# Kernel tuning notes

Hardware: AMD Instinct MI355X
Metric: run time of the kernel (lower is better)

Reference implementation:

```python
import jax, jax.numpy as jnp
import numpy as np

PAD = 0

def setup_inputs() -> dict:
    key = jax.random.key(0)
    k1, k2, k3, k4 = jax.random.split(key, 4)
    B, S, F, V, H, D = 64, 256, 4, 50257, 768, 512
    words = jax.random.randint(k1, (B, S, F), 0, V, dtype=jnp.int64)  # pad_index=0 occurs rarely at random
    E = jax.random.normal(k2, (V, H), dtype=jnp.float32) * 0.02      # stand-in for transformer last_hidden_state producer
    W = jax.random.normal(k3, (H, D), dtype=jnp.float32) * 0.02      # FFN projection weight
    b = jax.random.normal(k4, (D,), dtype=jnp.float32) * 0.02
    return {"words": words, "E": E, "W": W, "b": b}

def reference(words, E, W, b):
    # words: [B, S, F] subword ids; mask out pad subwords
    mask = (words != PAD)                                  # [B,S,F] bool
    sub = E[words] * mask[..., None].astype(E.dtype)       # [B,S,F,H], pads zeroed
    cnt = mask.sum(-1).astype(E.dtype)                     # [B,S] subwords per word
    # segment-mean over the fix_len axis; fully-padded words -> 0 (matches pad_sequence(..., 0))
    word_emb = sub.sum(-2) / jnp.maximum(cnt, 1.0)[..., None]   # [B,S,H]
    word_emb = jnp.where((cnt > 0)[..., None], word_emb, 0.0)
    return word_emb @ W + b                                # [B,S,D]
```

## Files before the change

### kernel.cpp

```cpp
#include <hip/hip_runtime.h>
#include <hip/hip_bf16.h>

#define M_TOT 16384
#define K_TOT 768
#define N_TOT 512
#define BM 16
#define NT 12
#define NSLOT 96

typedef __attribute__((ext_vector_type(8))) __bf16 bf16x8;
typedef __attribute__((ext_vector_type(4))) float f32x4;

static __device__ __forceinline__ ushort f2bf(float x) {
  union { float f; unsigned int u; } v; v.f = x;
  unsigned int r = v.u + 0x7fffu + ((v.u >> 16) & 1u);
  return (ushort)(r >> 16);
}
static __device__ __forceinline__ unsigned pack2(float lo, float hi) {
  return (unsigned)f2bf(lo) | ((unsigned)f2bf(hi) << 16);
}

__global__ __launch_bounds__(256) void wt_kernel(const float* __restrict__ W,
                                                 ushort* __restrict__ Wt) {
  __shared__ float tile[64][65];
  const int t  = threadIdx.x;
  const int k0 = blockIdx.x * 64;
  const int n0 = blockIdx.y * 64;
#pragma unroll
  for (int i = 0; i < 4; ++i) {
    const int idx = t + i * 256;
    const int r = idx >> 4;
    const int c = (idx & 15) * 4;
    const float4 v =
        *reinterpret_cast<const float4*>(W + (size_t)(k0 + r) * N_TOT + n0 + c);
    tile[r][c + 0] = v.x; tile[r][c + 1] = v.y;
    tile[r][c + 2] = v.z; tile[r][c + 3] = v.w;
  }
  __syncthreads();
#pragma unroll
  for (int i = 0; i < 4; ++i) {
    const int idx = t + i * 256;
    const int rn = idx >> 4;
    const int ck = (idx & 15) * 4;
    ushort4 o;
    o.x = f2bf(tile[ck + 0][rn]);
    o.y = f2bf(tile[ck + 1][rn]);
    o.z = f2bf(tile[ck + 2][rn]);
    o.w = f2bf(tile[ck + 3][rn]);
    const int kg    = k0 + ck;
    const int chunk = kg >> 3;
    const int e0    = kg & 7;
    *reinterpret_cast<ushort4*>(
        &Wt[((size_t)chunk * N_TOT + n0 + rn) * 8 + e0]) = o;
  }
}

__global__ __launch_bounds__(256) void fused_kernel(
    const int* __restrict__ words, const float* __restrict__ E,
    const ushort* __restrict__ Wt, const float* __restrict__ bias,
    float* __restrict__ out) {
  __shared__ ushort A_l[BM * NSLOT * 8];
  __shared__ int   eoff_l[BM][4];
  __shared__ float msk_l[BM][4];
  __shared__ float scl_l[BM];

  const int t    = threadIdx.x;
  const int lane = t & 63;
  const int w    = t >> 6;
  const int bm   = blockIdx.x;

  if (t < BM) {
    const int4 w4 =
        *reinterpret_cast<const int4*>(words + (size_t)(bm * BM + t) * 4);
    const int ids[4] = {w4.x, w4.y, w4.z, w4.w};
    float cnt = 0.f;
#pragma unroll
    for (int f = 0; f < 4; ++f) {
      eoff_l[t][f] = ids[f] * K_TOT;
      const float m = (ids[f] != 0) ? 1.f : 0.f;
      msk_l[t][f] = m;
      cnt += m;
    }
    scl_l[t] = (cnt > 0.f) ? (1.f / cnt) : 0.f;
  }
  __syncthreads();

  const int sr  = t >> 4;
  const int c16 = t & 15;
  const float4* pf[4];
#pragma unroll
  for (int f = 0; f < 4; ++f)
    pf[f] = reinterpret_cast<const float4*>(E + eoff_l[sr][f]);
  const float m0 = msk_l[sr][0], m1 = msk_l[sr][1];
  const float m2 = msk_l[sr][2], m3 = msk_l[sr][3];
  const float scl = scl_l[sr];

  float4 vgA[8], vgB[8];

#define G_LOAD(vg, g)                                                        \
  do {                                                                       \
    const int s_ = c16 + 16 * (g);                                           \
    _Pragma("unroll") for (int f = 0; f < 4; ++f) {                          \
      vg[2 * f + 0] = pf[f][s_ * 2 + 0];                                     \
      vg[2 * f + 1] = pf[f][s_ * 2 + 1];                                     \
    }                                                                        \
  } while (0)

#define G_MATH(vg, g)                                                        \
  do {                                                                       \
    const int s_  = c16 + 16 * (g);                                          \
    const int kt_ = s_ >> 3;                                                 \
    const int sw_ = (s_ & 7) ^ (sr & 7);                                     \
    float s[8];                                                              \
    _Pragma("unroll") for (int j = 0; j < 4; ++j) {                          \
      s[j] = (vg[0][j] * m0 + vg[2][j] * m1 + vg[4][j] * m2 + vg[6][j] * m3) \
             * scl;                                                          \
      s[4 + j] =                                                             \
          (vg[1][j] * m0 + vg[3][j] * m1 + vg[5][j] * m2 + vg[7][j] * m3) *  \
          scl;                                                               \
    }                                                                        \
    uint4 o;                                                                 \
    o.x = pack2(s[0], s[1]); o.y = pack2(s[2], s[3]);                        \
    o.z = pack2(s[4], s[5]); o.w = pack2(s[6], s[7]);                        \
    *reinterpret_cast<uint4*>(                                               \
        &A_l[(sr * NSLOT + kt_ * 8 + sw_) * 8]) = o;                         \
  } while (0)

  G_LOAD(vgA, 0);  G_LOAD(vgB, 1);
  G_MATH(vgA, 0);  G_LOAD(vgA, 2);
  G_MATH(vgB, 1);  G_LOAD(vgB, 3);
  G_MATH(vgA, 2);  G_LOAD(vgA, 4);
  G_MATH(vgB, 3);  G_LOAD(vgB, 5);
  G_MATH(vgA, 4);
  G_MATH(vgB, 5);
#undef G_LOAD
#undef G_MATH
  __syncthreads();

  f32x4 acc[8];
#pragma unroll
  for (int n = 0; n < 8; ++n) acc[n] = (f32x4){0.f, 0.f, 0.f, 0.f};

  const int rsel = lane & 15;
  const int ksel = lane >> 4;
  const int colBase = w * 128 + rsel;

#pragma unroll
  for (int kt = 0; kt < NT; ++kt) {
#pragma unroll
    for (int kk = 0; kk < 2; ++kk) {
      const int ks = kk * 4 + ksel;
      const bf16x8 af = *reinterpret_cast<const bf16x8*>(
          &A_l[(rsel * NSLOT + kt * 8 + (ks ^ (rsel & 7))) * 8]);
      bf16x8 bfr[8];
#pragma unroll
      for (int n = 0; n < 8; ++n)
        bfr[n] = *reinterpret_cast<const bf16x8*>(
            &Wt[((size_t)(kt * 8 + ks) * N_TOT + colBase + n * 16) * 8]);
      __builtin_amdgcn_s_setprio(1);
#pragma unroll
      for (int n = 0; n < 8; ++n)
        acc[n] = __builtin_amdgcn_mfma_f32_16x16x32_bf16(af, bfr[n], acc[n],
                                                         0, 0, 0);
      __builtin_amdgcn_s_setprio(0);
    }
  }

  const int row0 = bm * BM + (ksel << 2);
#pragma unroll
  for (int n = 0; n < 8; ++n) {
    const float bv = bias[colBase + n * 16];
#pragma unroll
    for (int j = 0; j < 4; ++j) {
      __builtin_nontemporal_store(
          acc[n][j] + bv,
          &out[(size_t)(row0 + j) * N_TOT + colBase + n * 16]);
    }
  }
}

extern "C" void kernel_launch(void* const* d_in, const int* in_sizes, int n_in,
                              void* d_out, int out_size, void* d_ws,
                              size_t ws_size, hipStream_t stream) {
  const int*   words = (const int*)d_in[0];
  const float* E     = (const float*)d_in[1];
  const float* W     = (const float*)d_in[2];
  const float* b     = (const float*)d_in[3];
  float* out = (float*)d_out;

  ushort* Wtws = (ushort*)d_ws;

  hipLaunchKernelGGL(wt_kernel, dim3(K_TOT / 64, N_TOT / 64), dim3(256), 0,
                     stream, W, Wtws);
  hipLaunchKernelGGL(fused_kernel, dim3(M_TOT / BM), dim3(256), 0, stream,
                     words, E, Wtws, b, out);
}
```

Before: 64.41 us.

## Enlarge row tile to 64 with 512-thread blocks for W fragment reuse

Raises the M tile from 16 to 64 rows and doubles the block to 8 waves. The gather is reorganised so each wave loads 8 full embedding rows with lane-contiguous float4 reads. In the GEMM each wave computes a 64x64 output tile, using 4x4 MFMA accumulators. Each loaded W fragment is now reused across four row tiles, which cuts global and L2 traffic for Wt. In exchange the grid shrinks to 256 blocks and LDS use grows to about 96KB per block, which limits residency and may leave fewer gather loads in flight to hide latency.

```diff
diff --git a/kernel.cpp b/kernel.cpp
--- a/kernel.cpp
+++ b/kernel.cpp
@@ -4,9 +4,8 @@
 #define M_TOT 16384
 #define K_TOT 768
 #define N_TOT 512
-#define BM 16
+#define BM 64
 #define NT 12
-#define NSLOT 96
 
 typedef __attribute__((ext_vector_type(8))) __bf16 bf16x8;
 typedef __attribute__((ext_vector_type(4))) float f32x4;
@@ -55,11 +54,11 @@
   }
 }
 
-__global__ __launch_bounds__(256) void fused_kernel(
+__global__ __launch_bounds__(512, 2) void fused_kernel(
     const int* __restrict__ words, const float* __restrict__ E,
     const ushort* __restrict__ Wt, const float* __restrict__ bias,
     float* __restrict__ out) {
-  __shared__ ushort A_l[BM * NSLOT * 8];
+  __shared__ ushort A_l[BM * 96 * 8];
   __shared__ int   eoff_l[BM][4];
   __shared__ float msk_l[BM][4];
   __shared__ float scl_l[BM];
@@ -85,96 +84,103 @@
   }
   __syncthreads();
 
-  const int sr  = t >> 4;
-  const int c16 = t & 15;
-  const float4* pf[4];
-#pragma unroll
-  for (int f = 0; f < 4; ++f)
-    pf[f] = reinterpret_cast<const float4*>(E + eoff_l[sr][f]);
-  const float m0 = msk_l[sr][0], m1 = msk_l[sr][1];
-  const float m2 = msk_l[sr][2], m3 = msk_l[sr][3];
-  const float scl = scl_l[sr];
-
-  float4 vgA[8], vgB[8];
-
-#define G_LOAD(vg, g)                                                        \
+  const int rbase = w * 8;
+  float4 vA[12], vB[12];
+
+#define G_LOAD(vv, r)                                                        \
   do {                                                                       \
-    const int s_ = c16 + 16 * (g);                                           \
+    const int row_ = rbase + (r);                                            \
     _Pragma("unroll") for (int f = 0; f < 4; ++f) {                          \
-      vg[2 * f + 0] = pf[f][s_ * 2 + 0];                                     \
-      vg[2 * f + 1] = pf[f][s_ * 2 + 1];                                     \
+      const float4* p_ =                                                     \
+          reinterpret_cast<const float4*>(E + eoff_l[row_][f]) + lane;       \
+      vv[f * 3 + 0] = p_[0];                                                 \
+      vv[f * 3 + 1] = p_[64];                                                \
+      vv[f * 3 + 2] = p_[128];                                               \
     }                                                                        \
   } while (0)
 
-#define G_MATH(vg, g)                                                        \
+#define G_MATH(vv, r)                                                        \
   do {                                                                       \
-    const int s_  = c16 + 16 * (g);                                          \
-    const int kt_ = s_ >> 3;                                                 \
-    const int sw_ = (s_ & 7) ^ (sr & 7);                                     \
-    float s[8];                                                              \
-    _Pragma("unroll") for (int j = 0; j < 4; ++j) {                          \
-      s[j] = (vg[0][j] * m0 + vg[2][j] * m1 + vg[4][j] * m2 + vg[6][j] * m3) \
-             * scl;                                                          \
-      s[4 + j] =                                                             \
-          (vg[1][j] * m0 + vg[3][j] * m1 + vg[5][j] * m2 + vg[7][j] * m3) *  \
-          scl;                                                               \
+    const int row_ = rbase + (r);                                            \
+    const float km0 = msk_l[row_][0], km1 = msk_l[row_][1];                  \
+    const float km2 = msk_l[row_][2], km3 = msk_l[row_][3];                  \
+    const float ksc = scl_l[row_];                                           \
+    _Pragma("unroll") for (int c = 0; c < 3; ++c) {                          \
+      float s[4];                                                            \
+      _Pragma("unroll") for (int j = 0; j < 4; ++j)                          \
+        s[j] = (vv[0 * 3 + c][j] * km0 + vv[1 * 3 + c][j] * km1 +            \
+                vv[2 * 3 + c][j] * km2 + vv[3 * 3 + c][j] * km3) * ksc;      \
+      uint2 o_;                                                              \
+      o_.x = pack2(s[0], s[1]);                                              \
+      o_.y = pack2(s[2], s[3]);                                              \
+      const int slot_ = c * 32 + ((lane >> 1) ^ (r));   \
+      *reinterpret_cast<uint2*>(                                             \
+          &A_l[row_ * 768 + slot_ * 8 + (lane & 1) * 4]) = o_;               \
     }                                                                        \
-    uint4 o;                                                                 \
-    o.x = pack2(s[0], s[1]); o.y = pack2(s[2], s[3]);                        \
-    o.z = pack2(s[4], s[5]); o.w = pack2(s[6], s[7]);                        \
-    *reinterpret_cast<uint4*>(                                               \
-        &A_l[(sr * NSLOT + kt_ * 8 + sw_) * 8]) = o;                         \
   } while (0)
 
-  G_LOAD(vgA, 0);  G_LOAD(vgB, 1);
-  G_MATH(vgA, 0);  G_LOAD(vgA, 2);
-  G_MATH(vgB, 1);  G_LOAD(vgB, 3);
-  G_MATH(vgA, 2);  G_LOAD(vgA, 4);
-  G_MATH(vgB, 3);  G_LOAD(vgB, 5);
-  G_MATH(vgA, 4);
-  G_MATH(vgB, 5);
+  G_LOAD(vA, 0);  G_LOAD(vB, 1);
+  G_MATH(vA, 0);  G_LOAD(vA, 2);
+  G_MATH(vB, 1);  G_LOAD(vB, 3);
+  G_MATH(vA, 2);  G_LOAD(vA, 4);
+  G_MATH(vB, 3);  G_LOAD(vB, 5);
+  G_MATH(vA, 4);  G_LOAD(vA, 6);
+  G_MATH(vB, 5);  G_LOAD(vB, 7);
+  G_MATH(vA, 6);
+  G_MATH(vB, 7);
 #undef G_LOAD
 #undef G_MATH
   __syncthreads();
 
-  f32x4 acc[8];
-#pragma unroll
-  for (int n = 0; n < 8; ++n) acc[n] = (f32x4){0.f, 0.f, 0.f, 0.f};
+  f32x4 acc[4][4];
+#pragma unroll
+  for (int m = 0; m < 4; ++m)
+#pragma unroll
+    for (int n = 0; n < 4; ++n) acc[m][n] = (f32x4){0.f, 0.f, 0.f, 0.f};
 
   const int rsel = lane & 15;
   const int ksel = lane >> 4;
-  const int colBase = w * 128 + rsel;
+  const int colBase = w * 64 + rsel;
 
 #pragma unroll
   for (int kt = 0; kt < NT; ++kt) {
 #pragma unroll
     for (int kk = 0; kk < 2; ++kk) {
-      const int ks = kk * 4 + ksel;
-      const bf16x8 af = *reinterpret_cast<const bf16x8*>(
-          &A_l[(rsel * NSLOT + kt * 8 + (ks ^ (rsel & 7))) * 8]);
-      bf16x8 bfr[8];
-#pragma unroll
-      for (int n = 0; n < 8; ++n)
+      const int g = kt * 8 + kk * 4 + ksel;
+      bf16x8 af[4], bfr[4];
+#pragma unroll
+      for (int m = 0; m < 4; ++m) {
+        const int r_ = m * 16 + rsel;
+        af[m] = *reinterpret_cast<const bf16x8*>(
+            &A_l[r_ * 768 + (g ^ (r_ & 7)) * 8]);
+      }
+#pragma unroll
+      for (int n = 0; n < 4; ++n)
         bfr[n] = *reinterpret_cast<const bf16x8*>(
-            &Wt[((size_t)(kt * 8 + ks) * N_TOT + colBase + n * 16) * 8]);
+            &Wt[((size_t)g * N_TOT + colBase + n * 16) * 8]);
       __builtin_amdgcn_s_setprio(1);
 #pragma unroll
-      for (int n = 0; n < 8; ++n)
-        acc[n] = __builtin_amdgcn_mfma_f32_16x16x32_bf16(af, bfr[n], acc[n],
-                                                         0, 0, 0);
+      for (int m = 0; m < 4; ++m)
+#pragma unroll
+        for (int n = 0; n < 4; ++n)
+          acc[m][n] = __builtin_amdgcn_mfma_f32_16x16x32_bf16(
+              af[m], bfr[n], acc[m][n], 0, 0, 0);
       __builtin_amdgcn_s_setprio(0);
     }
   }
 
   const int row0 = bm * BM + (ksel << 2);
 #pragma unroll
-  for (int n = 0; n < 8; ++n) {
+  for (int n = 0; n < 4; ++n) {
     const float bv = bias[colBase + n * 16];
 #pragma unroll
-    for (int j = 0; j < 4; ++j) {
-      __builtin_nontemporal_store(
-          acc[n][j] + bv,
-          &out[(size_t)(row0 + j) * N_TOT + colBase + n * 16]);
+    for (int m = 0; m < 4; ++m) {
+#pragma unroll
+      for (int j = 0; j < 4; ++j) {
+        __builtin_nontemporal_store(
+            acc[m][n][j] + bv,
+            &out[(size_t)(row0 + m * 16 + j) * N_TOT + colBase + n * 16]);
+      }
     }
   }
 }
@@ -192,6 +198,6 @@
 
   hipLaunchKernelGGL(wt_kernel, dim3(K_TOT / 64, N_TOT / 64), dim3(256), 0,
                      stream, W, Wtws);
-  hipLaunchKernelGGL(fused_kernel, dim3(M_TOT / BM), dim3(256), 0, stream,
+  hipLaunchKernelGGL(fused_kernel, dim3(M_TOT / BM), dim3(512), 0, stream,
                      words, E, Wtws, b, out);
 }
```

Result: faster. 54.97 us (-14.7%).
